# Optimization experiments

Measured on AMD Instinct MI355X. Metric: run time of the kernel, lower is better.

Reference implementation:

```python
import jax, jax.numpy as jnp
import numpy as np

B, C, H, W = 8, 512, 64, 64
CQ = C // 8  # query/key projection dim


def setup_inputs() -> dict:
    key = jax.random.key(0)
    ks = jax.random.split(key, 8)
    s = 0.02
    return {
        "x": jax.random.normal(ks[0], (B, C, H, W), dtype=jnp.float32),
        "Wq": jax.random.normal(ks[1], (CQ, C), dtype=jnp.float32) * s,
        "bq": jax.random.normal(ks[2], (CQ,), dtype=jnp.float32) * s,
        "Wk": jax.random.normal(ks[3], (CQ, C), dtype=jnp.float32) * s,
        "bk": jax.random.normal(ks[4], (CQ,), dtype=jnp.float32) * s,
        "Wv": jax.random.normal(ks[5], (C, C), dtype=jnp.float32) * s,
        "bv": jax.random.normal(ks[6], (C,), dtype=jnp.float32) * s,
        "gamma": jax.random.normal(ks[7], (1,), dtype=jnp.float32) * 0.1,
    }


def reference(x, Wq, bq, Wk, bk, Wv, bv, gamma):
    b, c, h, w = x.shape
    n = h * w
    xf = x.reshape(b, c, n)                                  # [B,C,N]
    # 1x1 convs == per-pixel linear maps over channels
    q = jnp.einsum('dc,bcn->bdn', Wq, xf) + bq[:, None]       # [B,CQ,N]
    k = jnp.einsum('dc,bcn->bdn', Wk, xf) + bk[:, None]       # [B,CQ,N]
    v = jnp.einsum('dc,bcn->bdn', Wv, xf) + bv[:, None]       # [B,C,N]
    # attention[b, i, j] = softmax_j( q_i . k_j )
    attn = jax.nn.softmax(jnp.einsum('bdn,bdm->bnm', q, k), axis=-1)  # [B,N,N]
    # out[b, c, i] = sum_j v[b, c, j] * attn[b, i, j]
    out = jnp.einsum('bcj,bij->bci', v, attn).reshape(b, c, h, w)
    return gamma[0] * out + x
```

## Files before the change

kernel.cpp:

```cpp
#include <hip/hip_runtime.h>
#include <hip/hip_bf16.h>

#define BB 8
#define CC 512
#define NN 4096
#define CQ 64

typedef __bf16 bf16;
typedef __bf16 bf16x4 __attribute__((ext_vector_type(4)));
typedef __bf16 bf16x8 __attribute__((ext_vector_type(8)));
typedef float f32x4 __attribute__((ext_vector_type(4)));

__device__ __forceinline__ f32x4 mfma16(bf16x8 a, bf16x8 b, f32x4 c) {
    return __builtin_amdgcn_mfma_f32_16x16x32_bf16(a, b, c, 0, 0, 0);
}

#define BAR_LDS()                                            \
    do {                                                     \
        asm volatile("s_waitcnt lgkmcnt(0)" ::: "memory");   \
        __builtin_amdgcn_s_barrier();                        \
    } while (0)


__global__ __launch_bounds__(256) void k_transpose(const float* __restrict__ x,
                                                   bf16* __restrict__ xTt) {
    __shared__ float tile[64][65];
    const int b  = blockIdx.z;
    const int c0 = blockIdx.y * 64;
    const int n0 = blockIdx.x * 64;
    const int t  = threadIdx.x;

    const float* xp = x + ((size_t)b * CC + c0) * NN + n0;
#pragma unroll
    for (int r = 0; r < 16; ++r) {
        int c = r * 4 + (t >> 6);
        int n = t & 63;
        tile[c][n] = xp[(size_t)c * NN + n];
    }
    __syncthreads();
#pragma unroll
    for (int r = 0; r < 16; ++r) {
        int nl = r * 4 + (t >> 6);
        int cl = t & 63;
        size_t off = ((size_t)(b * 256 + (n0 >> 4) + (nl >> 4)) * 16 + (c0 >> 5) + (cl >> 5)) * 512
                   + (nl & 15) * 32 + (cl & 31);
        xTt[off] = (bf16)tile[cl][nl];
    }
}

__global__ __launch_bounds__(256) void k_castw(const float* __restrict__ Wq,
                                               const float* __restrict__ Wk,
                                               const float* __restrict__ Wv,
                                               bf16* __restrict__ Wqt,
                                               bf16* __restrict__ Wkt,
                                               bf16* __restrict__ Wvt) {
    int i = blockIdx.x * 256 + threadIdx.x;
    const int nqk = CQ * CC;
    const float* src;
    bf16* dst;
    int j;
    if (i < nqk) {
        src = Wq; dst = Wqt; j = i;
    } else if (i < 2 * nqk) {
        src = Wk; dst = Wkt; j = i - nqk;
    } else if (i < 2 * nqk + CC * CC) {
        src = Wv; dst = Wvt; j = i - 2 * nqk;
    } else {
        return;
    }
    int d = j >> 9;
    int c = j & 511;
    size_t off = ((size_t)(d >> 4) * 16 + (c >> 5)) * 512 + (d & 15) * 32 + (c & 31);
    dst[off] = (bf16)src[j];
}

__global__ __launch_bounds__(256, 2) void k_proj(const bf16* __restrict__ xTt,
                                                 const bf16* __restrict__ Wvt,
                                                 const bf16* __restrict__ Wqt,
                                                 const bf16* __restrict__ Wkt,
                                                 const float* __restrict__ bv,
                                                 const float* __restrict__ bq,
                                                 const float* __restrict__ bk,
                                                 bf16* __restrict__ vt,
                                                 bf16* __restrict__ qTt,
                                                 bf16* __restrict__ kTt) {
    const int b  = blockIdx.y;
    const int bx = blockIdx.x;
    const int w  = threadIdx.x >> 6;
    const int l  = threadIdx.x & 63;
    const int l15 = l & 15, lq = l >> 4;
    const int loff = l15 * 32 + lq * 8;

    const bf16* bp = xTt + ((size_t)(b * 256 + bx * 4) * 16) * 512 + loff;

    {
        f32x4 acc[8][4];
#pragma unroll
        for (int dt = 0; dt < 8; ++dt) {
            f32x4 binit;
#pragma unroll
            for (int r = 0; r < 4; ++r) binit[r] = bv[(w * 8 + dt) * 16 + lq * 4 + r];
#pragma unroll
            for (int nt = 0; nt < 4; ++nt) acc[dt][nt] = binit;
        }

        const bf16* ap = Wvt + ((size_t)(w * 8) * 16) * 512 + loff;
#pragma unroll 1
        for (int ct = 0; ct < 16; ++ct) {
            bf16x8 bxf[4];
#pragma unroll
            for (int nt = 0; nt < 4; ++nt)
                bxf[nt] = *(const bf16x8*)(bp + ((size_t)nt * 16 + ct) * 512);
#pragma unroll
            for (int dt = 0; dt < 8; ++dt) {
                bf16x8 aW = *(const bf16x8*)(ap + ((size_t)dt * 16 + ct) * 512);
#pragma unroll
                for (int nt = 0; nt < 4; ++nt)
                    acc[dt][nt] = mfma16(aW, bxf[nt], acc[dt][nt]);
            }
        }
#pragma unroll
        for (int dt = 0; dt < 8; ++dt) {
#pragma unroll
            for (int nt = 0; nt < 4; ++nt) {
#pragma unroll
                for (int r = 0; r < 4; ++r) {
                    size_t off = ((size_t)(b * 32 + w * 8 + dt) * 128 + bx * 2 + (nt >> 1)) * 512
                               + (lq * 4 + r) * 32 + (nt & 1) * 16 + l15;
                    vt[off] = (bf16)acc[dt][nt][r];
                }
            }
        }
    }

    {
        f32x4 aq[4], ak[4];
        {
            float bvq = bq[w * 16 + l15];
            float bvk = bk[w * 16 + l15];
#pragma unroll
            for (int nt = 0; nt < 4; ++nt) {
                aq[nt] = (f32x4){bvq, bvq, bvq, bvq};
                ak[nt] = (f32x4){bvk, bvk, bvk, bvk};
            }
        }
#pragma unroll 2
        for (int ct = 0; ct < 16; ++ct) {
            bf16x8 fq = *(const bf16x8*)(Wqt + ((size_t)w * 16 + ct) * 512 + loff);
            bf16x8 fk = *(const bf16x8*)(Wkt + ((size_t)w * 16 + ct) * 512 + loff);
#pragma unroll
            for (int nt = 0; nt < 4; ++nt) {
                bf16x8 bxf = *(const bf16x8*)(bp + ((size_t)nt * 16 + ct) * 512);
                aq[nt] = mfma16(bxf, fq, aq[nt]);
                ak[nt] = mfma16(bxf, fk, ak[nt]);
            }
        }
#pragma unroll
        for (int nt = 0; nt < 4; ++nt) {
#pragma unroll
            for (int r = 0; r < 4; ++r) {
                size_t off = ((size_t)(b * 256 + bx * 4 + nt) * 2 + (w >> 1)) * 512
                           + (lq * 4 + r) * 32 + (w & 1) * 16 + l15;
                qTt[off] = (bf16)aq[nt][r];
                kTt[off] = (bf16)ak[nt][r];
            }
        }
    }
}

__global__ __launch_bounds__(512, 2) void k_attn(const bf16* __restrict__ qTt,
                                                 const bf16* __restrict__ kTt,
                                                 const bf16* __restrict__ vt,
                                                 const float* __restrict__ x,
                                                 const float* __restrict__ gamma,
                                                 float* __restrict__ out) {
    __shared__ bf16  Pl[2][8][1024];
    __shared__ bf16  Kl[2][8][512];
    __shared__ float Ll[8][16];

    const int b  = blockIdx.x & 7;
    const int i0 = (blockIdx.x >> 3) * 128;
    const int t  = threadIdx.x;
    const int w  = t >> 6;
    const int l  = t & 63;
    const int l15 = l & 15, lq = l >> 4;
    const int loff = l15 * 32 + lq * 8;

    const f32x4 zero4 = {0.f, 0.f, 0.f, 0.f};

    const bf16* kb = kTt + (size_t)b * 256 * 2 * 512;
    const bf16* qb = qTt + (size_t)b * 256 * 2 * 512;
    const bf16* vb = vt + ((size_t)b * 32 + w * 4) * 128 * 512 + loff;

    bf16x8 qa0, qa1;
    {
        const bf16* qp = qb + ((size_t)((i0 >> 4) + w) * 2) * 512 + loff;
        qa0 = *(const bf16x8*)qp;
        qa1 = *(const bf16x8*)(qp + 512);
    }

    f32x4 acc[4][8];
#pragma unroll
    for (int ct = 0; ct < 4; ++ct)
#pragma unroll
        for (int it = 0; it < 8; ++it) acc[ct][it] = zero4;
    float lsum = 0.f;

    bf16x8 kcur;
    {
        bf16x8 k0 = *(const bf16x8*)(kb + (size_t)w * 512 + loff);
        *(bf16x8*)&Kl[0][w][l * 8] = k0;
        kcur = *(const bf16x8*)(kb + (size_t)(8 + w) * 512 + loff);
    }
    BAR_LDS();

#pragma unroll 2
    for (int jb = 0; jb < NN / 64; ++jb) {
        const int buf = jb & 1;

        bf16x8 va[4][2];
#pragma unroll
        for (int ct = 0; ct < 4; ++ct)
#pragma unroll
            for (int h = 0; h < 2; ++h)
                va[ct][h] = *(const bf16x8*)(vb + ((size_t)ct * 128 + jb * 2 + h) * 512);

        bf16x8 knxt;
        {
            const int jk = (jb + 2) & (NN / 64 - 1);
            knxt = *(const bf16x8*)(kb + ((size_t)jk * 8 + w) * 512 + loff);
        }

        bf16x8 ka[8];
#pragma unroll
        for (int q = 0; q < 8; ++q)
            ka[q] = *(const bf16x8*)&Kl[buf][q][l * 8];

        f32x4 st[4];
#pragma unroll
        for (int jt = 0; jt < 4; ++jt) {
            f32x4 s = mfma16(ka[jt * 2], qa0, zero4);
            st[jt] = mfma16(ka[jt * 2 + 1], qa1, s);
        }

        *(bf16x8*)&Kl[buf ^ 1][w][l * 8] = kcur;
        kcur = knxt;

#pragma unroll
        for (int jt = 0; jt < 4; ++jt) {
            float p0 = __expf(st[jt][0]);
            float p1 = __expf(st[jt][1]);
            float p2 = __expf(st[jt][2]);
            float p3 = __expf(st[jt][3]);
            lsum += (p0 + p1) + (p2 + p3);
            bf16x4 pk = {(bf16)p0, (bf16)p1, (bf16)p2, (bf16)p3};
            int g = jt * 2 + (lq >> 1);
            *(bf16x4*)&Pl[buf][w][g * 128 + l15 * 8 + (lq & 1) * 4] = pk;
        }

        BAR_LDS();

        __builtin_amdgcn_s_setprio(1);
        bf16x8 pA = *(const bf16x8*)&Pl[buf][0][l * 8];
        bf16x8 pB = *(const bf16x8*)&Pl[buf][0][512 + l * 8];
#pragma unroll
        for (int it = 0; it < 8; ++it) {
            bf16x8 nA, nB;
            if (it < 7) {
                nA = *(const bf16x8*)&Pl[buf][it + 1][l * 8];
                nB = *(const bf16x8*)&Pl[buf][it + 1][512 + l * 8];
            }
            acc[0][it] = mfma16(va[0][0], pA, acc[0][it]);
            acc[1][it] = mfma16(va[1][0], pA, acc[1][it]);
            acc[2][it] = mfma16(va[2][0], pA, acc[2][it]);
            acc[3][it] = mfma16(va[3][0], pA, acc[3][it]);
            acc[0][it] = mfma16(va[0][1], pB, acc[0][it]);
            acc[1][it] = mfma16(va[1][1], pB, acc[1][it]);
            acc[2][it] = mfma16(va[2][1], pB, acc[2][it]);
            acc[3][it] = mfma16(va[3][1], pB, acc[3][it]);
            pA = nA;
            pB = nB;
        }
        __builtin_amdgcn_s_setprio(0);
    }

    lsum += __shfl_xor(lsum, 16);
    lsum += __shfl_xor(lsum, 32);
    if (l < 16) Ll[w][l] = lsum;
    __syncthreads();

    const float g = gamma[0];
    float linv[8];
#pragma unroll
    for (int it = 0; it < 8; ++it) linv[it] = 1.0f / Ll[it][l15];

#pragma unroll
    for (int ct = 0; ct < 4; ++ct) {
#pragma unroll
        for (int it = 0; it < 8; ++it) {
#pragma unroll
            for (int r = 0; r < 4; ++r) {
                int c = (w * 4 + ct) * 16 + lq * 4 + r;
                size_t idx = ((size_t)b * CC + c) * NN + i0 + it * 16 + l15;
                out[idx] = g * (acc[ct][it][r] * linv[it]) + x[idx];
            }
        }
    }
}

extern "C" void kernel_launch(void* const* d_in, const int* in_sizes, int n_in,
                              void* d_out, int out_size, void* d_ws, size_t ws_size,
                              hipStream_t stream) {
    const float* x     = (const float*)d_in[0];
    const float* Wq    = (const float*)d_in[1];
    const float* bq    = (const float*)d_in[2];
    const float* Wk    = (const float*)d_in[3];
    const float* bk    = (const float*)d_in[4];
    const float* Wv    = (const float*)d_in[5];
    const float* bv    = (const float*)d_in[6];
    const float* gamma = (const float*)d_in[7];
    float* out = (float*)d_out;

    char* p = (char*)d_ws;
    bf16* xTt = (bf16*)p; p += (size_t)BB * NN * CC * sizeof(bf16);
    bf16* qTt = (bf16*)p; p += (size_t)BB * NN * CQ * sizeof(bf16);
    bf16* kTt = (bf16*)p; p += (size_t)BB * NN * CQ * sizeof(bf16);
    bf16* vt  = (bf16*)p; p += (size_t)BB * CC * NN * sizeof(bf16);
    bf16* Wqt = (bf16*)p; p += (size_t)CQ * CC * sizeof(bf16);
    bf16* Wkt = (bf16*)p; p += (size_t)CQ * CC * sizeof(bf16);
    bf16* Wvt = (bf16*)p; p += (size_t)CC * CC * sizeof(bf16);

    k_transpose<<<dim3(NN / 64, CC / 64, BB), 256, 0, stream>>>(x, xTt);
    k_castw<<<(2 * CQ * CC + CC * CC + 255) / 256, 256, 0, stream>>>(Wq, Wk, Wv, Wqt, Wkt, Wvt);
    k_proj<<<dim3(NN / 64, BB), 256, 0, stream>>>(xTt, Wvt, Wqt, Wkt, bv, bq, bk, vt, qTt, kTt);
    k_attn<<<256, 512, 0, stream>>>(qTt, kTt, vt, x, gamma, out);
}
```

Measured before the change: 203.7 us.

## Fuse x transpose/cast into projection kernel with double-buffered LDS staging

Removes the separate transpose kernel and its bf16 xTt workspace. The projection kernel now reads fp32 x directly, converts it to bf16 and transposes it through a double-buffered LDS tile while prefetching the next channel chunks. The Q/K and V projections are merged into one loop so each x tile is loaded once. This saves a full write and read of the transposed activation and one launch, at the cost of more barriers and extra register pressure in the fused loop.

```diff
diff --git a/kernel.cpp b/kernel.cpp
--- a/kernel.cpp
+++ b/kernel.cpp
@@ -21,32 +21,6 @@
         __builtin_amdgcn_s_barrier();                        \
     } while (0)
 
-
-__global__ __launch_bounds__(256) void k_transpose(const float* __restrict__ x,
-                                                   bf16* __restrict__ xTt) {
-    __shared__ float tile[64][65];
-    const int b  = blockIdx.z;
-    const int c0 = blockIdx.y * 64;
-    const int n0 = blockIdx.x * 64;
-    const int t  = threadIdx.x;
-
-    const float* xp = x + ((size_t)b * CC + c0) * NN + n0;
-#pragma unroll
-    for (int r = 0; r < 16; ++r) {
-        int c = r * 4 + (t >> 6);
-        int n = t & 63;
-        tile[c][n] = xp[(size_t)c * NN + n];
-    }
-    __syncthreads();
-#pragma unroll
-    for (int r = 0; r < 16; ++r) {
-        int nl = r * 4 + (t >> 6);
-        int cl = t & 63;
-        size_t off = ((size_t)(b * 256 + (n0 >> 4) + (nl >> 4)) * 16 + (c0 >> 5) + (cl >> 5)) * 512
-                   + (nl & 15) * 32 + (cl & 31);
-        xTt[off] = (bf16)tile[cl][nl];
-    }
-}
 
 __global__ __launch_bounds__(256) void k_castw(const float* __restrict__ Wq,
                                                const float* __restrict__ Wk,
@@ -74,16 +48,18 @@
     dst[off] = (bf16)src[j];
 }
 
-__global__ __launch_bounds__(256, 2) void k_proj(const bf16* __restrict__ xTt,
-                                                 const bf16* __restrict__ Wvt,
-                                                 const bf16* __restrict__ Wqt,
-                                                 const bf16* __restrict__ Wkt,
-                                                 const float* __restrict__ bv,
-                                                 const float* __restrict__ bq,
-                                                 const float* __restrict__ bk,
-                                                 bf16* __restrict__ vt,
-                                                 bf16* __restrict__ qTt,
-                                                 bf16* __restrict__ kTt) {
+__global__ __launch_bounds__(256, 2) void k_projf(const float* __restrict__ x,
+                                                  const bf16* __restrict__ Wvt,
+                                                  const bf16* __restrict__ Wqt,
+                                                  const bf16* __restrict__ Wkt,
+                                                  const float* __restrict__ bv,
+                                                  const float* __restrict__ bq,
+                                                  const float* __restrict__ bk,
+                                                  bf16* __restrict__ vt,
+                                                  bf16* __restrict__ qTt,
+                                                  bf16* __restrict__ kTt) {
+    __shared__ bf16 XT[2][64][40];
+
     const int b  = blockIdx.y;
     const int bx = blockIdx.x;
     const int w  = threadIdx.x >> 6;
@@ -91,79 +67,99 @@
     const int l15 = l & 15, lq = l >> 4;
     const int loff = l15 * 32 + lq * 8;
 
-    const bf16* bp = xTt + ((size_t)(b * 256 + bx * 4) * 16) * 512 + loff;
-
+    const float* xb = x + (size_t)b * CC * NN + bx * 64 + l;
+
+    f32x4 acc[8][4];
+#pragma unroll
+    for (int dt = 0; dt < 8; ++dt) {
+        f32x4 binit;
+#pragma unroll
+        for (int r = 0; r < 4; ++r) binit[r] = bv[(w * 8 + dt) * 16 + lq * 4 + r];
+#pragma unroll
+        for (int nt = 0; nt < 4; ++nt) acc[dt][nt] = binit;
+    }
+    f32x4 aq[4], ak[4];
     {
-        f32x4 acc[8][4];
+        float bvq = bq[w * 16 + l15];
+        float bvk = bk[w * 16 + l15];
+#pragma unroll
+        for (int nt = 0; nt < 4; ++nt) {
+            aq[nt] = (f32x4){bvq, bvq, bvq, bvq};
+            ak[nt] = (f32x4){bvk, bvk, bvk, bvk};
+        }
+    }
+
+    auto LOADC = [&](int ct) {
+        bf16x8 pk;
+#pragma unroll
+        for (int r = 0; r < 8; ++r)
+            pk[r] = (bf16)xb[(size_t)(ct * 32 + w * 8 + r) * NN];
+        return pk;
+    };
+
+    {
+        bf16x8 c0 = LOADC(0);
+        *(bf16x8*)&XT[0][l][w * 8] = c0;
+    }
+    bf16x8 cnxt = LOADC(1);
+    BAR_LDS();
+
+#pragma unroll 2
+    for (int ct = 0; ct < 16; ++ct) {
+        const int buf = ct & 1;
+
+        bf16x8 c2;
+        if (ct < 14) c2 = LOADC(ct + 2);
+
+        bf16x8 bxf[4];
+#pragma unroll
+        for (int nt = 0; nt < 4; ++nt)
+            bxf[nt] = *(const bf16x8*)&XT[buf][nt * 16 + l15][lq * 8];
+
 #pragma unroll
         for (int dt = 0; dt < 8; ++dt) {
-            f32x4 binit;
-#pragma unroll
-            for (int r = 0; r < 4; ++r) binit[r] = bv[(w * 8 + dt) * 16 + lq * 4 + r];
-#pragma unroll
-            for (int nt = 0; nt < 4; ++nt) acc[dt][nt] = binit;
-        }
-
-        const bf16* ap = Wvt + ((size_t)(w * 8) * 16) * 512 + loff;
-#pragma unroll 1
-        for (int ct = 0; ct < 16; ++ct) {
-            bf16x8 bxf[4];
+            bf16x8 aW = *(const bf16x8*)(Wvt + ((size_t)(w * 8 + dt) * 16 + ct) * 512 + loff);
 #pragma unroll
             for (int nt = 0; nt < 4; ++nt)
-                bxf[nt] = *(const bf16x8*)(bp + ((size_t)nt * 16 + ct) * 512);
-#pragma unroll
-            for (int dt = 0; dt < 8; ++dt) {
-                bf16x8 aW = *(const bf16x8*)(ap + ((size_t)dt * 16 + ct) * 512);
-#pragma unroll
-                for (int nt = 0; nt < 4; ++nt)
-                    acc[dt][nt] = mfma16(aW, bxf[nt], acc[dt][nt]);
-            }
-        }
-#pragma unroll
-        for (int dt = 0; dt < 8; ++dt) {
-#pragma unroll
-            for (int nt = 0; nt < 4; ++nt) {
-#pragma unroll
-                for (int r = 0; r < 4; ++r) {
-                    size_t off = ((size_t)(b * 32 + w * 8 + dt) * 128 + bx * 2 + (nt >> 1)) * 512
-                               + (lq * 4 + r) * 32 + (nt & 1) * 16 + l15;
-                    vt[off] = (bf16)acc[dt][nt][r];
-                }
-            }
-        }
-    }
-
-    {
-        f32x4 aq[4], ak[4];
+                acc[dt][nt] = mfma16(aW, bxf[nt], acc[dt][nt]);
+        }
         {
-            float bvq = bq[w * 16 + l15];
-            float bvk = bk[w * 16 + l15];
-#pragma unroll
-            for (int nt = 0; nt < 4; ++nt) {
-                aq[nt] = (f32x4){bvq, bvq, bvq, bvq};
-                ak[nt] = (f32x4){bvk, bvk, bvk, bvk};
-            }
-        }
-#pragma unroll 2
-        for (int ct = 0; ct < 16; ++ct) {
             bf16x8 fq = *(const bf16x8*)(Wqt + ((size_t)w * 16 + ct) * 512 + loff);
             bf16x8 fk = *(const bf16x8*)(Wkt + ((size_t)w * 16 + ct) * 512 + loff);
 #pragma unroll
             for (int nt = 0; nt < 4; ++nt) {
-                bf16x8 bxf = *(const bf16x8*)(bp + ((size_t)nt * 16 + ct) * 512);
-                aq[nt] = mfma16(bxf, fq, aq[nt]);
-                ak[nt] = mfma16(bxf, fk, ak[nt]);
+                aq[nt] = mfma16(bxf[nt], fq, aq[nt]);
+                ak[nt] = mfma16(bxf[nt], fk, ak[nt]);
             }
         }
+
+        if (ct < 15)
+            *(bf16x8*)&XT[buf ^ 1][l][w * 8] = cnxt;
+        cnxt = c2;
+
+        BAR_LDS();
+    }
+
+#pragma unroll
+    for (int dt = 0; dt < 8; ++dt) {
 #pragma unroll
         for (int nt = 0; nt < 4; ++nt) {
 #pragma unroll
             for (int r = 0; r < 4; ++r) {
-                size_t off = ((size_t)(b * 256 + bx * 4 + nt) * 2 + (w >> 1)) * 512
-                           + (lq * 4 + r) * 32 + (w & 1) * 16 + l15;
-                qTt[off] = (bf16)aq[nt][r];
-                kTt[off] = (bf16)ak[nt][r];
+                size_t off = ((size_t)(b * 32 + w * 8 + dt) * 128 + bx * 2 + (nt >> 1)) * 512
+                           + (lq * 4 + r) * 32 + (nt & 1) * 16 + l15;
+                vt[off] = (bf16)acc[dt][nt][r];
             }
+        }
+    }
+#pragma unroll
+    for (int nt = 0; nt < 4; ++nt) {
+#pragma unroll
+        for (int r = 0; r < 4; ++r) {
+            size_t off = ((size_t)(b * 256 + bx * 4 + nt) * 2 + (w >> 1)) * 512
+                       + (lq * 4 + r) * 32 + (w & 1) * 16 + l15;
+            qTt[off] = (bf16)aq[nt][r];
+            kTt[off] = (bf16)ak[nt][r];
         }
     }
 }
@@ -322,7 +318,6 @@
     float* out = (float*)d_out;
 
     char* p = (char*)d_ws;
-    bf16* xTt = (bf16*)p; p += (size_t)BB * NN * CC * sizeof(bf16);
     bf16* qTt = (bf16*)p; p += (size_t)BB * NN * CQ * sizeof(bf16);
     bf16* kTt = (bf16*)p; p += (size_t)BB * NN * CQ * sizeof(bf16);
     bf16* vt  = (bf16*)p; p += (size_t)BB * CC * NN * sizeof(bf16);
@@ -330,8 +325,7 @@
     bf16* Wkt = (bf16*)p; p += (size_t)CQ * CC * sizeof(bf16);
     bf16* Wvt = (bf16*)p; p += (size_t)CC * CC * sizeof(bf16);
 
-    k_transpose<<<dim3(NN / 64, CC / 64, BB), 256, 0, stream>>>(x, xTt);
     k_castw<<<(2 * CQ * CC + CC * CC + 255) / 256, 256, 0, stream>>>(Wq, Wk, Wv, Wqt, Wkt, Wvt);
-    k_proj<<<dim3(NN / 64, BB), 256, 0, stream>>>(xTt, Wvt, Wqt, Wkt, bv, bq, bk, vt, qTt, kTt);
+    k_projf<<<dim3(NN / 64, BB), 256, 0, stream>>>(x, Wvt, Wqt, Wkt, bv, bq, bk, vt, qTt, kTt);
     k_attn<<<256, 512, 0, stream>>>(qTt, kTt, vt, x, gamma, out);
 }
```

New measurement: 188.1 us, median of 3. -7.7%, faster.
